# Performance work log

Hardware: AMD Instinct MI355X
Metric: run time of the kernel (lower is better)

## Reference

```python
import jax, jax.numpy as jnp
import numpy as np

B, D = 16384, 512
NUM_CLASSES, K = 90, 32


def _l2norm(v, axis=-1):
    return v / jnp.sqrt(jnp.sum(v * v, axis=axis, keepdims=True) + 1e-12)


def setup_inputs() -> dict:
    key = jax.random.key(0)
    k1, k2, k3 = jax.random.split(key, 3)
    x = jax.random.normal(k1, (B, D), dtype=jnp.float32)
    labels = jax.random.randint(k2, (B,), 0, NUM_CLASSES, dtype=jnp.int64)
    centers = jax.random.normal(k3, (NUM_CLASSES, K, D), dtype=jnp.float32)
    return {"x": x, "labels": labels, "centers": centers}


def reference(x, labels, centers):
    # l2Norm applied to centers at init and to x in forward
    xn = _l2norm(x, axis=1)                       # [B, D]
    cn = _l2norm(centers, axis=-1)                # [C, K, D]
    c = cn[labels]                                # gather: [B, K, D]
    # dst_k = 1 - <x_b, center_{label_b, k}>
    dst = 1.0 - jnp.einsum("bd,bkd->bk", xn, c)   # [B, K]
    score = jax.nn.softmax(2.0 - dst, axis=1)     # softmax over K sub-centers
    per_sample = jnp.sum(score * dst, axis=1)     # [B]
    return jnp.mean(per_sample)                   # scalar loss
```

## Files before the change

kernel.cpp:

```cpp
#include <hip/hip_runtime.h>
#include <hip/hip_bf16.h>

#define BB 16384
#define DD 512
#define NCLS 90
#define KC 32
#define BUCKET 512
#define PRB 180

typedef __attribute__((ext_vector_type(8))) short short8;
typedef __attribute__((ext_vector_type(4))) float fx4;

static __device__ __forceinline__ short f2bf(float f) {
    unsigned u = __float_as_uint(f);
    unsigned r = (u + 0x7fffu + ((u >> 16) & 1u)) >> 16;
    return (short)r;
}

static __device__ __forceinline__ void gload_lds16(const void* g, void* l) {
    __builtin_amdgcn_global_load_lds(
        (const __attribute__((address_space(1))) void*)g,
        (__attribute__((address_space(3))) void*)l, 16, 0, 0);
}

__global__ __launch_bounds__(1024)
void k_prep(const float* __restrict__ centers, const int* __restrict__ labels,
            short* __restrict__ cni, int* __restrict__ idx, int* __restrict__ cnt) {
    __shared__ int lab[BB];
    __shared__ int wcnt[16];

    int t = threadIdx.x, w = t >> 6, lane = t & 63;

    if ((int)blockIdx.x < PRB) {
        int row = blockIdx.x * 16 + w;
        const float4* p = (const float4*)(centers + (size_t)row * DD);
        float4 a = p[lane * 2];
        float4 b = p[lane * 2 + 1];
        float s = a.x * a.x + a.y * a.y + a.z * a.z + a.w * a.w
                + b.x * b.x + b.y * b.y + b.z * b.z + b.w * b.w;
#pragma unroll
        for (int m = 1; m < 64; m <<= 1) s += __shfl_xor(s, m, 64);
        float sc = rsqrtf(s + 1e-12f);
        short8 v;
        v[0] = f2bf(a.x * sc); v[1] = f2bf(a.y * sc);
        v[2] = f2bf(a.z * sc); v[3] = f2bf(a.w * sc);
        v[4] = f2bf(b.x * sc); v[5] = f2bf(b.y * sc);
        v[6] = f2bf(b.z * sc); v[7] = f2bf(b.w * sc);
        *(short8*)(cni + (size_t)row * DD + lane * 8) = v;
    } else {
        int c = blockIdx.x - PRB;
        for (int j = t; j < BB / 4; j += 1024)
            ((int4*)lab)[j] = ((const int4*)labels)[j];
        __syncthreads();

        int seg4 = w * (BB / 4 / 16);
        int cw = 0;
#pragma unroll
        for (int jj = 0; jj < 4; jj++) {
            int4 v = ((int4*)lab)[seg4 + jj * 64 + lane];
            cw += (v.x == c) + (v.y == c) + (v.z == c) + (v.w == c);
        }
#pragma unroll
        for (int m = 1; m < 64; m <<= 1) cw += __shfl_xor(cw, m, 64);
        if (lane == 0) wcnt[w] = cw;
        __syncthreads();
        int pos = c * BUCKET;
        for (int ww = 0; ww < w; ww++) pos += wcnt[ww];
#pragma unroll
        for (int jj = 0; jj < 4; jj++) {
            int4 v = ((int4*)lab)[seg4 + jj * 64 + lane];
            int gbase = (seg4 + jj * 64 + lane) * 4;
            {
                bool m = (v.x == c); unsigned long long k = __ballot(m);
                if (m) idx[pos + __popcll(k & ((1ull << lane) - 1ull))] = gbase + 0;
                pos += __popcll(k);
            }
            {
                bool m = (v.y == c); unsigned long long k = __ballot(m);
                if (m) idx[pos + __popcll(k & ((1ull << lane) - 1ull))] = gbase + 1;
                pos += __popcll(k);
            }
            {
                bool m = (v.z == c); unsigned long long k = __ballot(m);
                if (m) idx[pos + __popcll(k & ((1ull << lane) - 1ull))] = gbase + 2;
                pos += __popcll(k);
            }
            {
                bool m = (v.w == c); unsigned long long k = __ballot(m);
                if (m) idx[pos + __popcll(k & ((1ull << lane) - 1ull))] = gbase + 3;
                pos += __popcll(k);
            }
        }
        if (t == 0) {
            int s = 0;
#pragma unroll
            for (int i = 0; i < 16; i++) s += wcnt[i];
            cnt[c] = s;
        }
    }
}

__launch_bounds__(256, 2)
__global__ void k_main(const float* __restrict__ x,
                       const short* __restrict__ cni,
                       const int* __restrict__ cnt,
                       const int* __restrict__ idx,
                       float* __restrict__ partials) {
    __shared__ __align__(16) short c_lds[KC * DD];
    __shared__ __align__(16) short x_lds[32 * DD];
    __shared__ float S_lds[32][33];
    __shared__ float xinv[32];
    __shared__ float red[256];

    int c = blockIdx.x >> 3;
    int p = blockIdx.x & 7;
    int n = cnt[c];
    int nch = (n + 31) >> 5;
    int t = threadIdx.x, w = t >> 6, lane = t & 63;
    float loss_acc = 0.f;

    if (p < nch) {
        const short* cbase = cni + (size_t)c * KC * DD;
#pragma unroll
        for (int it = 0; it < 8; it++) {
            int q = t + 256 * it;
            int drow = q >> 6, cc = q & 63;
            int scc = cc ^ (drow & 7);
            gload_lds16(cbase + drow * DD + scc * 8, &c_lds[q * 8]);
        }

        int base = c * BUCKET;
        int mrow = ((w & 1) << 4) + (lane & 15);
        int nrow = ((w >> 1) << 4) + (lane & 15);
        int row8 = t >> 3, l8 = t & 7;

        for (int ch = p; ch < nch; ch += 8) {
            int off = ch << 5;
            int rem = n - off;

            {
                int r = (row8 < rem) ? row8 : (rem - 1);
                int g = idx[base + off + r];
                const float4* src = (const float4*)(x + (size_t)g * DD);
                float nrm = 0.f;
#pragma unroll
                for (int jj = 0; jj < 8; jj++) {
                    int cc = l8 + 8 * jj;
                    float4 a = src[cc * 2], b = src[cc * 2 + 1];
                    nrm += a.x * a.x + a.y * a.y + a.z * a.z + a.w * a.w
                         + b.x * b.x + b.y * b.y + b.z * b.z + b.w * b.w;
                    short8 v;
                    v[0] = f2bf(a.x); v[1] = f2bf(a.y); v[2] = f2bf(a.z); v[3] = f2bf(a.w);
                    v[4] = f2bf(b.x); v[5] = f2bf(b.y); v[6] = f2bf(b.z); v[7] = f2bf(b.w);
                    *(short8*)&x_lds[row8 * DD + ((cc ^ (row8 & 7)) << 3)] = v;
                }
#pragma unroll
                for (int m = 1; m < 8; m <<= 1) nrm += __shfl_xor(nrm, m, 64);
                if (l8 == 0) xinv[row8] = rsqrtf(nrm + 1e-12f);
            }
            __syncthreads();

            fx4 acc = {0.f, 0.f, 0.f, 0.f};
#pragma unroll
            for (int ks = 0; ks < 16; ks++) {
                int c16a = ks * 4 + (lane >> 4);
                short8 av = *(const short8*)&x_lds[mrow * DD + ((c16a ^ (mrow & 7)) << 3)];
                short8 bv = *(const short8*)&c_lds[nrow * DD + ((c16a ^ (nrow & 7)) << 3)];
                acc = __builtin_amdgcn_mfma_f32_16x16x32_bf16(av, bv, acc, 0, 0, 0);
            }
#pragma unroll
            for (int j = 0; j < 4; j++) {
                int r = ((w & 1) << 4) + ((lane >> 4) << 2) + j;
                int col = ((w >> 1) << 4) + (lane & 15);
                S_lds[r][col] = acc[j];
            }
            __syncthreads();

            {
                float xv = xinv[row8];
                int q4 = l8 << 2;
                float s0 = S_lds[row8][q4 + 0] * xv;
                float s1 = S_lds[row8][q4 + 1] * xv;
                float s2 = S_lds[row8][q4 + 2] * xv;
                float s3 = S_lds[row8][q4 + 3] * xv;
                float mx = fmaxf(fmaxf(s0, s1), fmaxf(s2, s3));
#pragma unroll
                for (int m = 1; m < 8; m <<= 1) mx = fmaxf(mx, __shfl_xor(mx, m, 64));
                float e0 = expf(s0 - mx), e1 = expf(s1 - mx);
                float e2 = expf(s2 - mx), e3 = expf(s3 - mx);
                float Z = e0 + e1 + e2 + e3;
                float num = e0 * (1.f - s0) + e1 * (1.f - s1)
                          + e2 * (1.f - s2) + e3 * (1.f - s3);
#pragma unroll
                for (int m = 1; m < 8; m <<= 1) {
                    Z += __shfl_xor(Z, m, 64);
                    num += __shfl_xor(num, m, 64);
                }
                if (l8 == 0 && row8 < rem) loss_acc += num / Z;
            }
            __syncthreads();
        }
    }

    red[t] = loss_acc;
    __syncthreads();
    for (int h = 128; h > 0; h >>= 1) {
        if (t < h) red[t] += red[t + h];
        __syncthreads();
    }
    if (t == 0) partials[blockIdx.x] = red[0];
}

__global__ void k_final(const float* __restrict__ partials, float* __restrict__ out) {
    __shared__ float red[256];
    int t = threadIdx.x;
    float s = 0.f;
    for (int i = t; i < NCLS * 8; i += 256) s += partials[i];
    red[t] = s;
    __syncthreads();
    for (int h = 128; h > 0; h >>= 1) {
        if (t < h) red[t] += red[t + h];
        __syncthreads();
    }
    if (t == 0) out[0] = red[0] * (1.0f / (float)BB);
}

extern "C" void kernel_launch(void* const* d_in, const int* in_sizes, int n_in,
                              void* d_out, int out_size, void* d_ws, size_t ws_size,
                              hipStream_t stream) {
    const float* x       = (const float*)d_in[0];
    const int*   labels  = (const int*)d_in[1];
    const float* centers = (const float*)d_in[2];
    float* out = (float*)d_out;

    char* ws = (char*)d_ws;
    short* cni      = (short*)(ws + 0);
    int*   idx      = (int*)(ws + 3145728);
    int*   cnt      = (int*)(ws + 3407872);
    float* partials = (float*)(ws + 3473408);

    k_prep<<<PRB + NCLS, 1024, 0, stream>>>(centers, labels, cni, idx, cnt);
    k_main<<<NCLS * 8, 256, 0, stream>>>(x, cni, cnt, idx, partials);
    k_final<<<1, 256, 0, stream>>>(partials, out);
}
```

Before: 28.69 us.

## Stream fp32 x rows into LDS asynchronously and split K across waves

The main kernel now gathers x rows with direct global-to-LDS 16-byte loads into a swizzled fp32 buffer instead of loading through registers. It converts them to bf16 with the packed intrinsic at MFMA operand time and fuses the norm computation into the K loop. Tiles shrink from 32 to 16 rows with the K dimension split across wave pairs, and the partial scores are summed in LDS. Each class gets 12 slices instead of 8 for more parallelism, and the trailing barrier per chunk is dropped. The trade-off is more LDS traffic for fp32 x reads and a 2-way partial-sum reduction.

```diff
diff --git a/kernel.cpp b/kernel.cpp
--- a/kernel.cpp
+++ b/kernel.cpp
@@ -7,6 +7,7 @@
 #define KC 32
 #define BUCKET 512
 #define PRB 180
+#define NSL 12
 
 typedef __attribute__((ext_vector_type(8))) short short8;
 typedef __attribute__((ext_vector_type(4))) float fx4;
@@ -16,7 +17,14 @@
     unsigned r = (u + 0x7fffu + ((u >> 16) & 1u)) >> 16;
     return (short)r;
 }
-
+static __device__ __forceinline__ short8 pack8(float4 a, float4 b) {
+    union { __hip_bfloat162 h[4]; short8 s; } u;
+    u.h[0] = __float22bfloat162_rn(make_float2(a.x, a.y));
+    u.h[1] = __float22bfloat162_rn(make_float2(a.z, a.w));
+    u.h[2] = __float22bfloat162_rn(make_float2(b.x, b.y));
+    u.h[3] = __float22bfloat162_rn(make_float2(b.z, b.w));
+    return u.s;
+}
 static __device__ __forceinline__ void gload_lds16(const void* g, void* l) {
     __builtin_amdgcn_global_load_lds(
         (const __attribute__((address_space(1))) void*)g,
@@ -70,26 +78,14 @@
         for (int jj = 0; jj < 4; jj++) {
             int4 v = ((int4*)lab)[seg4 + jj * 64 + lane];
             int gbase = (seg4 + jj * 64 + lane) * 4;
-            {
-                bool m = (v.x == c); unsigned long long k = __ballot(m);
-                if (m) idx[pos + __popcll(k & ((1ull << lane) - 1ull))] = gbase + 0;
-                pos += __popcll(k);
-            }
-            {
-                bool m = (v.y == c); unsigned long long k = __ballot(m);
-                if (m) idx[pos + __popcll(k & ((1ull << lane) - 1ull))] = gbase + 1;
-                pos += __popcll(k);
-            }
-            {
-                bool m = (v.z == c); unsigned long long k = __ballot(m);
-                if (m) idx[pos + __popcll(k & ((1ull << lane) - 1ull))] = gbase + 2;
-                pos += __popcll(k);
-            }
-            {
-                bool m = (v.w == c); unsigned long long k = __ballot(m);
-                if (m) idx[pos + __popcll(k & ((1ull << lane) - 1ull))] = gbase + 3;
-                pos += __popcll(k);
-            }
+            { bool m = (v.x == c); unsigned long long k = __ballot(m);
+              if (m) idx[pos + __popcll(k & ((1ull << lane) - 1ull))] = gbase;     pos += __popcll(k); }
+            { bool m = (v.y == c); unsigned long long k = __ballot(m);
+              if (m) idx[pos + __popcll(k & ((1ull << lane) - 1ull))] = gbase + 1; pos += __popcll(k); }
+            { bool m = (v.z == c); unsigned long long k = __ballot(m);
+              if (m) idx[pos + __popcll(k & ((1ull << lane) - 1ull))] = gbase + 2; pos += __popcll(k); }
+            { bool m = (v.w == c); unsigned long long k = __ballot(m);
+              if (m) idx[pos + __popcll(k & ((1ull << lane) - 1ull))] = gbase + 3; pos += __popcll(k); }
         }
         if (t == 0) {
             int s = 0;
@@ -100,24 +96,24 @@
     }
 }
 
-__launch_bounds__(256, 2)
-__global__ void k_main(const float* __restrict__ x,
-                       const short* __restrict__ cni,
-                       const int* __restrict__ cnt,
-                       const int* __restrict__ idx,
-                       float* __restrict__ partials) {
+__global__ __launch_bounds__(256, 2)
+void k_main(const float* __restrict__ x,
+            const short* __restrict__ cni,
+            const int* __restrict__ cnt,
+            const int* __restrict__ idx,
+            float* __restrict__ partials) {
     __shared__ __align__(16) short c_lds[KC * DD];
-    __shared__ __align__(16) short x_lds[32 * DD];
-    __shared__ float S_lds[32][33];
-    __shared__ float xinv[32];
+    __shared__ __align__(16) float xf[16 * DD];
+    __shared__ float S[2][16][34];
+    __shared__ float xn2[2][16];
     __shared__ float red[256];
 
-    int c = blockIdx.x >> 3;
-    int p = blockIdx.x & 7;
+    int b = blockIdx.x;
+    int c = b / NSL, p = b % NSL;
     int n = cnt[c];
-    int nch = (n + 31) >> 5;
+    int nch = (n + 15) >> 4;
     int t = threadIdx.x, w = t >> 6, lane = t & 63;
-    float loss_acc = 0.f;
+    float loss = 0.f;
 
     if (p < nch) {
         const short* cbase = cni + (size_t)c * KC * DD;
@@ -125,97 +121,92 @@
         for (int it = 0; it < 8; it++) {
             int q = t + 256 * it;
             int drow = q >> 6, cc = q & 63;
-            int scc = cc ^ (drow & 7);
-            gload_lds16(cbase + drow * DD + scc * 8, &c_lds[q * 8]);
-        }
-
-        int base = c * BUCKET;
-        int mrow = ((w & 1) << 4) + (lane & 15);
-        int nrow = ((w >> 1) << 4) + (lane & 15);
-        int row8 = t >> 3, l8 = t & 7;
-
-        for (int ch = p; ch < nch; ch += 8) {
-            int off = ch << 5;
+            gload_lds16(cbase + drow * DD + (cc ^ (drow & 7)) * 8, &c_lds[q * 8]);
+        }
+
+        int r = lane & 15, g4 = lane >> 4;
+        int kh = w >> 1, chf = w & 1;
+        int nrow = (chf << 4) + r;
+        int srow = t >> 4, l16 = t & 15;
+
+        for (int ch = p; ch < nch; ch += NSL) {
+            int off = ch << 4;
             int rem = n - off;
 
+            int gi = 0;
+            if (lane < 4) {
+                int i = off + (w << 2) + lane; if (i > n - 1) i = n - 1;
+                gi = idx[c * BUCKET + i];
+            }
+#pragma unroll
+            for (int j = 0; j < 4; j++) {
+                int row = (w << 2) + j;
+                int g = __shfl(gi, j, 64);
+                const char* src = (const char*)(x + (size_t)g * DD);
+                int sl = (lane ^ (row & 7)) << 4;
+                gload_lds16(src + sl,        &xf[row * DD]);
+                gload_lds16(src + 1024 + sl, &xf[row * DD + 256]);
+            }
+            __syncthreads();
+
+            fx4 acc = {0.f, 0.f, 0.f, 0.f};
+            float nrm = 0.f;
+#pragma unroll
+            for (int ks = 0; ks < 8; ks++) {
+                int cq = (kh * 8 + ks) * 4 + g4;
+                int p0 = (2 * cq) ^ (r & 7);
+                int p1 = (2 * cq + 1) ^ (r & 7);
+                float4 a0 = *(const float4*)&xf[r * DD + p0 * 4];
+                float4 a1 = *(const float4*)&xf[r * DD + p1 * 4];
+                nrm += a0.x * a0.x + a0.y * a0.y + a0.z * a0.z + a0.w * a0.w
+                     + a1.x * a1.x + a1.y * a1.y + a1.z * a1.z + a1.w * a1.w;
+                short8 av = pack8(a0, a1);
+                short8 bv = *(const short8*)&c_lds[nrow * DD + ((cq ^ (nrow & 7)) << 3)];
+                acc = __builtin_amdgcn_mfma_f32_16x16x32_bf16(av, bv, acc, 0, 0, 0);
+            }
+            nrm += __shfl_xor(nrm, 16, 64);
+            nrm += __shfl_xor(nrm, 32, 64);
+            if (chf == 0 && g4 == 0) xn2[kh][r] = nrm;
+#pragma unroll
+            for (int j = 0; j < 4; j++)
+                S[kh][(g4 << 2) + j][(chf << 4) + r] = acc[j];
+            __syncthreads();
+
             {
-                int r = (row8 < rem) ? row8 : (rem - 1);
-                int g = idx[base + off + r];
-                const float4* src = (const float4*)(x + (size_t)g * DD);
-                float nrm = 0.f;
-#pragma unroll
-                for (int jj = 0; jj < 8; jj++) {
-                    int cc = l8 + 8 * jj;
-                    float4 a = src[cc * 2], b = src[cc * 2 + 1];
-                    nrm += a.x * a.x + a.y * a.y + a.z * a.z + a.w * a.w
-                         + b.x * b.x + b.y * b.y + b.z * b.z + b.w * b.w;
-                    short8 v;
-                    v[0] = f2bf(a.x); v[1] = f2bf(a.y); v[2] = f2bf(a.z); v[3] = f2bf(a.w);
-                    v[4] = f2bf(b.x); v[5] = f2bf(b.y); v[6] = f2bf(b.z); v[7] = f2bf(b.w);
-                    *(short8*)&x_lds[row8 * DD + ((cc ^ (row8 & 7)) << 3)] = v;
-                }
-#pragma unroll
-                for (int m = 1; m < 8; m <<= 1) nrm += __shfl_xor(nrm, m, 64);
-                if (l8 == 0) xinv[row8] = rsqrtf(nrm + 1e-12f);
-            }
-            __syncthreads();
-
-            fx4 acc = {0.f, 0.f, 0.f, 0.f};
-#pragma unroll
-            for (int ks = 0; ks < 16; ks++) {
-                int c16a = ks * 4 + (lane >> 4);
-                short8 av = *(const short8*)&x_lds[mrow * DD + ((c16a ^ (mrow & 7)) << 3)];
-                short8 bv = *(const short8*)&c_lds[nrow * DD + ((c16a ^ (nrow & 7)) << 3)];
-                acc = __builtin_amdgcn_mfma_f32_16x16x32_bf16(av, bv, acc, 0, 0, 0);
-            }
-#pragma unroll
-            for (int j = 0; j < 4; j++) {
-                int r = ((w & 1) << 4) + ((lane >> 4) << 2) + j;
-                int col = ((w >> 1) << 4) + (lane & 15);
-                S_lds[r][col] = acc[j];
-            }
-            __syncthreads();
-
-            {
-                float xv = xinv[row8];
-                int q4 = l8 << 2;
-                float s0 = S_lds[row8][q4 + 0] * xv;
-                float s1 = S_lds[row8][q4 + 1] * xv;
-                float s2 = S_lds[row8][q4 + 2] * xv;
-                float s3 = S_lds[row8][q4 + 3] * xv;
-                float mx = fmaxf(fmaxf(s0, s1), fmaxf(s2, s3));
-#pragma unroll
-                for (int m = 1; m < 8; m <<= 1) mx = fmaxf(mx, __shfl_xor(mx, m, 64));
-                float e0 = expf(s0 - mx), e1 = expf(s1 - mx);
-                float e2 = expf(s2 - mx), e3 = expf(s3 - mx);
-                float Z = e0 + e1 + e2 + e3;
-                float num = e0 * (1.f - s0) + e1 * (1.f - s1)
-                          + e2 * (1.f - s2) + e3 * (1.f - s3);
-#pragma unroll
-                for (int m = 1; m < 8; m <<= 1) {
-                    Z += __shfl_xor(Z, m, 64);
+                float xv = rsqrtf(xn2[0][srow] + xn2[1][srow] + 1e-12f);
+                int c0 = l16 * 2;
+                float sa = (S[0][srow][c0]     + S[1][srow][c0])     * xv;
+                float sb = (S[0][srow][c0 + 1] + S[1][srow][c0 + 1]) * xv;
+                float mx = fmaxf(sa, sb);
+#pragma unroll
+                for (int m = 1; m < 16; m <<= 1) mx = fmaxf(mx, __shfl_xor(mx, m, 64));
+                float ea = expf(sa - mx), eb = expf(sb - mx);
+                float Z = ea + eb;
+                float num = ea * (1.f - sa) + eb * (1.f - sb);
+#pragma unroll
+                for (int m = 1; m < 16; m <<= 1) {
+                    Z   += __shfl_xor(Z, m, 64);
                     num += __shfl_xor(num, m, 64);
                 }
-                if (l8 == 0 && row8 < rem) loss_acc += num / Z;
-            }
-            __syncthreads();
-        }
-    }
-
-    red[t] = loss_acc;
+                if (l16 == 0 && srow < rem) loss += num / Z;
+            }
+        }
+    }
+
+    red[t] = loss;
     __syncthreads();
     for (int h = 128; h > 0; h >>= 1) {
         if (t < h) red[t] += red[t + h];
         __syncthreads();
     }
-    if (t == 0) partials[blockIdx.x] = red[0];
+    if (t == 0) partials[b] = red[0];
 }
 
 __global__ void k_final(const float* __restrict__ partials, float* __restrict__ out) {
     __shared__ float red[256];
     int t = threadIdx.x;
     float s = 0.f;
-    for (int i = t; i < NCLS * 8; i += 256) s += partials[i];
+    for (int i = t; i < NCLS * NSL; i += 256) s += partials[i];
     red[t] = s;
     __syncthreads();
     for (int h = 128; h > 0; h >>= 1) {
@@ -240,6 +231,6 @@
     float* partials = (float*)(ws + 3473408);
 
     k_prep<<<PRB + NCLS, 1024, 0, stream>>>(centers, labels, cni, idx, cnt);
-    k_main<<<NCLS * 8, 256, 0, stream>>>(x, cni, cnt, idx, partials);
+    k_main<<<NCLS * NSL, 256, 0, stream>>>(x, cni, cnt, idx, partials);
     k_final<<<1, 256, 0, stream>>>(partials, out);
 }
```

Result: slower. 29.81 us (+3.9%).
